# Kernel optimization log

Hardware: AMD Instinct MI355X
Metric: run time of the kernel (lower is better)

## Reference

```python
import jax, jax.numpy as jnp
import numpy as np

N_NODES = 10000


def _sage_pool(h, src, dst, Wp, bp, Ws, Wn, b):
    # DGL SAGEConv 'pool': m = relu(fc_pool(h_src)); neigh = max over in-edges;
    # out = fc_self(h_dst) + fc_neigh(neigh) + bias. Zero-in-degree nodes get 0 neigh.
    m = jax.nn.relu(h @ Wp + bp)                      # [N, d_in] node-level transform
    neigh = jax.ops.segment_max(m[src], dst, num_segments=N_NODES)  # [N, d_in]
    neigh = jnp.where(jnp.isfinite(neigh), neigh, 0.0)  # empty segments filled -inf -> 0
    return h @ Ws + neigh @ Wn + b


def setup_inputs() -> dict:
    key = jax.random.key(0)
    ks = jax.random.split(key, 20)
    dims = [(960, 512), (512, 512), (512, 1)]
    inp = {
        "h": jax.random.normal(ks[0], (N_NODES, 960), dtype=jnp.float32),
        "src": jax.random.randint(ks[1], (160000,), 0, N_NODES),
        "dst": jax.random.randint(ks[2], (160000,), 0, N_NODES),
    }
    ki = 3
    for l, (di, do) in enumerate(dims):
        inp[f"Wp{l}"] = jax.random.normal(ks[ki + 0], (di, di), dtype=jnp.float32) * 0.02
        inp[f"bp{l}"] = jnp.zeros((di,), dtype=jnp.float32)
        inp[f"Ws{l}"] = jax.random.normal(ks[ki + 1], (di, do), dtype=jnp.float32) * 0.02
        inp[f"Wn{l}"] = jax.random.normal(ks[ki + 2], (di, do), dtype=jnp.float32) * 0.02
        inp[f"b{l}"] = jnp.zeros((do,), dtype=jnp.float32)
        ki += 3
    return inp


def reference(h, src, dst,
              Wp0, bp0, Ws0, Wn0, b0,
              Wp1, bp1, Ws1, Wn1, b1,
              Wp2, bp2, Ws2, Wn2, b2):
    # layer 0: 960 -> 512, relu (dropout = identity in eval)
    x = jax.nn.relu(_sage_pool(h, src, dst, Wp0, bp0, Ws0, Wn0, b0))
    # layer 1: 512 -> 512, relu
    x = jax.nn.relu(_sage_pool(x, src, dst, Wp1, bp1, Ws1, Wn1, b1))
    # layer 2: 512 -> 1, sigmoid, squeeze -> per-node prediction
    x = _sage_pool(x, src, dst, Wp2, bp2, Ws2, Wn2, b2)
    return jax.nn.sigmoid(x).squeeze(-1)  # [N]
```

## Files before the change

### kernel.cpp

```cpp
#include <hip/hip_runtime.h>
#include <stdint.h>

#define NN 10000
#define NE 160000
#define MPAD 10112
#define MTILES 79

typedef unsigned short u16;
typedef float f32x4 __attribute__((ext_vector_type(4)));
typedef short short8 __attribute__((ext_vector_type(8)));
typedef __bf16 bf16x8 __attribute__((ext_vector_type(8)));
typedef unsigned short u16x4 __attribute__((ext_vector_type(4)));
typedef unsigned short u16x8 __attribute__((ext_vector_type(8)));

__device__ __forceinline__ float bf2f(u16 u) {
  union { unsigned u; float f; } c; c.u = ((unsigned)u) << 16; return c.f;
}
__device__ __forceinline__ u16 f2bf(float f) {
  union { float f; unsigned u; } c; c.f = f;
  return (u16)((c.u + 0x7FFFu + ((c.u >> 16) & 1u)) >> 16);
}

__device__ __forceinline__ void gld_lds16(void* lds, const void* g) {
  __builtin_amdgcn_global_load_lds(
      (const unsigned int __attribute__((address_space(1)))*)g,
      (unsigned int __attribute__((address_space(3)))*)lds, 16, 0, 0);
}

__global__ __launch_bounds__(256) void deg_count(const int* __restrict__ dst, int* __restrict__ deg) {
  int e = blockIdx.x * 256 + threadIdx.x;
  if (e < NE) atomicAdd(&deg[dst[e]], 1);
}

__global__ __launch_bounds__(256) void scan_off(const int* __restrict__ deg,
                                                int* __restrict__ roff, int* __restrict__ cur) {
  __shared__ int sdeg[10240];
  __shared__ int part[256];
  const int t = threadIdx.x;
  for (int k = t; k < NN; k += 256) sdeg[k] = deg[k];
  for (int k = NN + t; k < 10240; k += 256) sdeg[k] = 0;
  __syncthreads();
  const int CH = 40;
  int s = 0;
#pragma unroll
  for (int i = 0; i < CH; ++i) s += sdeg[t * CH + i];
  part[t] = s; __syncthreads();
  for (int off = 1; off < 256; off <<= 1) {
    int v = (t >= off) ? part[t - off] : 0;
    __syncthreads(); part[t] += v; __syncthreads();
  }
  int run = (t == 0) ? 0 : part[t - 1];
#pragma unroll
  for (int i = 0; i < CH; ++i) {
    const int idx = t * CH + i;
    const int d = sdeg[idx];
    sdeg[idx] = run;
    run += d;
  }
  __syncthreads();
  for (int k = t; k < NN; k += 256) { const int v = sdeg[k]; roff[k] = v; cur[k] = v; }
  if (t == 255) roff[NN] = NE;
}

__global__ __launch_bounds__(256) void fill_csr(const int* __restrict__ src, const int* __restrict__ dst,
                                                int* __restrict__ cur, int* __restrict__ esrc) {
  int e = blockIdx.x * 256 + threadIdx.x;
  if (e < NE) {
    int p = atomicAdd(&cur[dst[e]], 1);
    esrc[p] = src[e];
  }
}

__global__ __launch_bounds__(256) void convert_h(const float* __restrict__ h, u16* __restrict__ hbf,
                                                 int* __restrict__ deg) {
  if (blockIdx.x < 40) {
    const int z = blockIdx.x * 256 + threadIdx.x;
    if (z < NN) deg[z] = 0;
  }
  const size_t i = (size_t)(blockIdx.x * 256 + threadIdx.x) * 4;
  if (i >= (size_t)MPAD * 960) return;
  u16x4 o;
  if (i < (size_t)NN * 960) {
    float4 v = *(const float4*)(h + i);
    o[0] = f2bf(v.x); o[1] = f2bf(v.y); o[2] = f2bf(v.z); o[3] = f2bf(v.w);
  } else {
    o[0] = 0; o[1] = 0; o[2] = 0; o[3] = 0;
  }
  *(u16x4*)(hbf + i) = o;
}

struct WDesc { const float* in; u16* out; int R, C, Cpad, ldo, koff; };
struct WPack { WDesc d[7]; };

__global__ __launch_bounds__(256) void transpose_all(WPack p) {
  const WDesc w = p.d[blockIdx.z];
  const int cb = blockIdx.x * 32, rb = blockIdx.y * 32;
  if (cb >= w.Cpad || rb >= w.R) return;
  __shared__ float tile[32][33];
  const int tx = threadIdx.x & 31, ty = threadIdx.x >> 5;
  for (int i = ty; i < 32; i += 8) {
    int r = rb + i, c = cb + tx;
    tile[i][tx] = (r < w.R && c < w.C) ? w.in[(size_t)r * w.C + c] : 0.f;
  }
  __syncthreads();
  for (int i = ty; i < 32; i += 8) {
    int c = cb + i, r = rb + tx;
    if (c < w.Cpad && r < w.R) w.out[(size_t)c * w.ldo + w.koff + r] = f2bf(tile[tx][i]);
  }
}

template<int TM, int TN, int MINW>
__global__ __launch_bounds__(512, MINW) void gemm3(
    const u16* __restrict__ A0, int lda0,
    const u16* __restrict__ A1, int lda1, int ksplit,
    const u16* __restrict__ B,
    const float* __restrict__ bias, int nbias,
    u16* __restrict__ Cb, int ldcb,
    int K, int act, int tiles_n) {
  constexpr int TR = TM + TN;
  constexpr int NC = TR * 128 / (512 * 16);
  constexpr int WCOLS = 4;
  constexpr int WN = TN / WCOLS;
  constexpr int NJ = WN / 16;
  constexpr int MT = MPAD / TM;
  __shared__ __align__(16) u16 S0[TR * 64];
  __shared__ __align__(16) u16 S1[TR * 64];
  const int tid = threadIdx.x;
  const int wave = tid >> 6, lane = tid & 63;

  const int nwg = tiles_n * MT;
  const int orig = blockIdx.x + blockIdx.y * tiles_n;
  const int q = nwg >> 3, r8 = nwg & 7;
  const int xcd = orig & 7, idx = orig >> 3;
  const int wg = (xcd < r8 ? xcd * (q + 1) : r8 * (q + 1) + (xcd - r8) * q) + idx;
  const int tm = (wg / tiles_n) * TM;
  const int tn = (wg % tiles_n) * TN;

  const int wr = (wave / WCOLS) * 64;
  const int wc = (wave % WCOLS) * WN;
  const int fr = lane & 15, fq = lane >> 4;
  const int sr8 = lane >> 3;
  const int sslot = lane & 7;
  f32x4 acc[4][NJ] = {};

  auto stage = [&](u16* Sw, int kk) {
#pragma unroll
    for (int c = 0; c < NC; ++c) {
      const int row = c * 64 + wave * 8 + sr8;
      const int gs = (sslot ^ (row & 7)) * 8;
      const void* g;
      if (c < NC * TM / TR) {
        g = (kk < ksplit)
            ? (const void*)&A0[(size_t)(tm + row) * lda0 + kk + gs]
            : (const void*)&A1[(size_t)(tm + row) * lda1 + (kk - ksplit) + gs];
      } else {
        g = (const void*)&B[(size_t)(tn + row - TM) * (size_t)K + kk + gs];
      }
      gld_lds16(&Sw[(c * 64 + wave * 8) * 64], g);
    }
  };

  const int nsteps = K >> 6;
  stage(S0, 0);
  stage(S1, 64);
  for (int base = 0; base < nsteps; base += 2) {
#pragma unroll
    for (int ph = 0; ph < 2; ++ph) {
      const int t = base + ph;
      if (t >= nsteps) break;
      u16* Sr = (ph == 0) ? S0 : S1;
      if (t + 1 < nsteps) {
        asm volatile("s_waitcnt vmcnt(%0)" :: "i"(NC) : "memory");
      } else {
        asm volatile("s_waitcnt vmcnt(0)" ::: "memory");
      }
      __builtin_amdgcn_s_barrier();
      __builtin_amdgcn_sched_barrier(0);
      short8 af[4][2], bfr[2][NJ];
#pragma unroll
      for (int i = 0; i < 4; ++i) {
        const int r = wr + i * 16 + fr;
#pragma unroll
        for (int kc = 0; kc < 2; ++kc)
          af[i][kc] = *(const short8*)&Sr[r * 64 + ((((kc << 2) | fq) ^ (r & 7)) << 3)];
      }
#pragma unroll
      for (int j = 0; j < NJ; ++j) {
        const int r = TM + wc + j * 16 + fr;
#pragma unroll
        for (int kc = 0; kc < 2; ++kc)
          bfr[kc][j] = *(const short8*)&Sr[r * 64 + ((((kc << 2) | fq) ^ (r & 7)) << 3)];
      }
      asm volatile("s_waitcnt lgkmcnt(0)" ::: "memory");
      __builtin_amdgcn_sched_barrier(0);
      __builtin_amdgcn_s_barrier();
      if (t + 2 < nsteps) stage(Sr, (t + 2) << 6);
      __builtin_amdgcn_s_setprio(1);
#pragma unroll
      for (int kc = 0; kc < 2; ++kc)
#pragma unroll
        for (int i = 0; i < 4; ++i)
#pragma unroll
          for (int j = 0; j < NJ; ++j)
            acc[i][j] = __builtin_amdgcn_mfma_f32_16x16x32_bf16(
                __builtin_bit_cast(bf16x8, af[i][kc]), __builtin_bit_cast(bf16x8, bfr[kc][j]),
                acc[i][j], 0, 0, 0);
      __builtin_amdgcn_s_setprio(0);
      __builtin_amdgcn_sched_barrier(0);
    }
  }

  const int cr = fq * 4, cc = fr;
#pragma unroll
  for (int i = 0; i < 4; ++i)
#pragma unroll
    for (int j = 0; j < NJ; ++j) {
      const int col = tn + wc + j * 16 + cc;
      const float bv = (col < nbias) ? bias[col] : 0.f;
#pragma unroll
      for (int r = 0; r < 4; ++r) {
        const int row = tm + wr + i * 16 + cr + r;
        float v = acc[i][j][r] + bv;
        if (act) v = fmaxf(v, 0.f);
        Cb[(size_t)row * ldcb + col] = f2bf(v);
      }
    }
}

template<int CW>
__global__ __launch_bounds__(256) void aggregate_xcd(
    const u16* __restrict__ m, int ldm, const int* __restrict__ roff,
    const int* __restrict__ esrc, u16* __restrict__ neigh, int ldn) {
  constexpr int TPN = CW / 8;
  constexpr int NPB = 256 / TPN;
  const int chunk = blockIdx.x & 7;
  const int node = (blockIdx.x >> 3) * NPB + threadIdx.x / TPN;
  if (node >= NN) return;
  const int fi = chunk * CW + (threadIdx.x % TPN) * 8;
  const int beg = roff[node], end = roff[node + 1];
  u16x8 a;
#pragma unroll
  for (int i = 0; i < 8; ++i) a[i] = 0;
  for (int e = beg; e < end; ++e) {
    const u16* row = m + (size_t)esrc[e] * ldm;
    u16x8 v = *(const u16x8*)(row + fi);
#pragma unroll
    for (int i = 0; i < 8; ++i) a[i] = (v[i] > a[i]) ? v[i] : a[i];
  }
  *(u16x8*)(neigh + (size_t)node * ldn + fi) = a;
}

__global__ __launch_bounds__(256) void agg_final(
    const u16* __restrict__ m, const int* __restrict__ roff,
    const int* __restrict__ esrc, const u16* __restrict__ x,
    const float* __restrict__ ws, const float* __restrict__ wn,
    const float* __restrict__ b, float* __restrict__ out) {
  const int wave = threadIdx.x >> 6, lane = threadIdx.x & 63;
  const int n = blockIdx.x * 4 + wave;
  if (n >= NN) return;
  const int f = lane * 8;
  const int beg = roff[n], end = roff[n + 1];
  u16x8 a;
#pragma unroll
  for (int i = 0; i < 8; ++i) a[i] = 0;
  for (int e = beg; e < end; ++e) {
    u16x8 v = *(const u16x8*)(m + (size_t)esrc[e] * 512 + f);
#pragma unroll
    for (int i = 0; i < 8; ++i) a[i] = (v[i] > a[i]) ? v[i] : a[i];
  }
  const u16x8 xv = *(const u16x8*)(x + (size_t)n * 512 + f);
  float s = 0.f;
#pragma unroll
  for (int i = 0; i < 8; ++i)
    s += bf2f(xv[i]) * ws[f + i] + bf2f(a[i]) * wn[f + i];
#pragma unroll
  for (int o = 32; o > 0; o >>= 1) s += __shfl_xor(s, o);
  if (lane == 0) out[n] = 1.f / (1.f + expf(-(s + b[0])));
}

extern "C" void kernel_launch(void* const* d_in, const int* in_sizes, int n_in,
                              void* d_out, int out_size, void* d_ws, size_t ws_size,
                              hipStream_t stream) {
  const float* h   = (const float*)d_in[0];
  const int*   src = (const int*)d_in[1];
  const int*   dst = (const int*)d_in[2];
  const float* Wp0 = (const float*)d_in[3];
  const float* bp0 = (const float*)d_in[4];
  const float* Ws0 = (const float*)d_in[5];
  const float* Wn0 = (const float*)d_in[6];
  const float* b0  = (const float*)d_in[7];
  const float* Wp1 = (const float*)d_in[8];
  const float* bp1 = (const float*)d_in[9];
  const float* Ws1 = (const float*)d_in[10];
  const float* Wn1 = (const float*)d_in[11];
  const float* b1  = (const float*)d_in[12];
  const float* Wp2 = (const float*)d_in[13];
  const float* bp2 = (const float*)d_in[14];
  const float* Ws2 = (const float*)d_in[15];
  const float* Wn2 = (const float*)d_in[16];
  const float* b2  = (const float*)d_in[17];
  float* out = (float*)d_out;

  char* ws = (char*)d_ws;
  size_t off = 0;
  auto alloc = [&](size_t n) { char* p = ws + off; off = (off + n + 255) & ~(size_t)255; return p; };
  u16* hbf   = (u16*)alloc((size_t)MPAD * 960 * 2);
  u16* x1    = (u16*)alloc((size_t)MPAD * 512 * 2);
  u16* x2    = (u16*)alloc((size_t)MPAD * 512 * 2);
  u16* mbuf  = (u16*)alloc((size_t)MPAD * 1024 * 2);
  u16* nbuf  = (u16*)alloc((size_t)MPAD * 1024 * 2);
  u16* WpT0  = (u16*)alloc((size_t)1024 * 960 * 2);
  u16* Bcat0 = (u16*)alloc((size_t)512 * 1920 * 2);
  u16* WpT1  = (u16*)alloc((size_t)512 * 512 * 2);
  u16* Bcat1 = (u16*)alloc((size_t)512 * 1024 * 2);
  u16* WpT2  = (u16*)alloc((size_t)512 * 512 * 2);
  int* deg   = (int*)alloc(NN * 4);
  int* roff  = (int*)alloc((NN + 1) * 4);
  int* curp  = (int*)alloc(NN * 4);
  int* esrc  = (int*)alloc(NE * 4);

  convert_h<<<(MPAD * 960 / 4) / 256, 256, 0, stream>>>(h, hbf, deg);
  deg_count<<<NE / 256, 256, 0, stream>>>(dst, deg);
  scan_off<<<1, 256, 0, stream>>>(deg, roff, curp);
  fill_csr<<<NE / 256, 256, 0, stream>>>(src, dst, curp, esrc);

  WPack wp;
  wp.d[0] = {Wp0, WpT0,  960, 960, 1024,  960,   0};
  wp.d[1] = {Ws0, Bcat0, 960, 512,  512, 1920,   0};
  wp.d[2] = {Wn0, Bcat0, 960, 512,  512, 1920, 960};
  wp.d[3] = {Wp1, WpT1,  512, 512,  512,  512,   0};
  wp.d[4] = {Ws1, Bcat1, 512, 512,  512, 1024,   0};
  wp.d[5] = {Wn1, Bcat1, 512, 512,  512, 1024, 512};
  wp.d[6] = {Wp2, WpT2,  512, 512,  512,  512,   0};
  transpose_all<<<dim3(32, 30, 7), 256, 0, stream>>>(wp);

  gemm3<128, 128, 4><<<dim3(8, 79), 512, 0, stream>>>(
      hbf, 960, hbf, 960, 960, WpT0, bp0, 960, mbuf, 1024, 960, 1, 8);
  aggregate_xcd<128><<<5000, 256, 0, stream>>>(mbuf, 1024, roff, esrc, nbuf, 1024);
  gemm3<128, 128, 4><<<dim3(4, 79), 512, 0, stream>>>(
      hbf, 960, nbuf, 1024, 960, Bcat0, b0, 512, x1, 512, 1920, 1, 4);

  gemm3<128, 128, 4><<<dim3(4, 79), 512, 0, stream>>>(
      x1, 512, x1, 512, 512, WpT1, bp1, 512, mbuf, 512, 512, 1, 4);
  aggregate_xcd<64><<<2504, 256, 0, stream>>>(mbuf, 512, roff, esrc, nbuf, 512);
  gemm3<128, 128, 4><<<dim3(4, 79), 512, 0, stream>>>(
      x1, 512, nbuf, 512, 512, Bcat1, b1, 512, x2, 512, 1024, 1, 4);

  gemm3<128, 128, 4><<<dim3(4, 79), 512, 0, stream>>>(
      x2, 512, x2, 512, 512, WpT2, bp2, 512, mbuf, 512, 512, 1, 4);
  agg_final<<<2500, 256, 0, stream>>>(mbuf, roff, esrc, x2, Ws2, Wn2, b2, out);
}
```

Before: 228.7 us.

## Fuse self-projection into pool GEMM and fold CSR fill into transpose kernel

Layers 0 and 1 now fold the self term h@Ws into the same GEMM as the pool transform by concatenating Wp and Ws along N. The extra column tiles write fp32 partials, and the neighbour GEMM adds them back in its epilogue, so that GEMM's K shrinks to just the neighbour dimension. The CSR fill is merged into transpose_all as an extra z-slice, which removes one launch. The cost is fp32 partial buffers that must be written and read again, plus a wider first GEMM grid.

```diff
diff --git a/kernel.cpp b/kernel.cpp
--- a/kernel.cpp
+++ b/kernel.cpp
@@ -62,15 +62,6 @@
   if (t == 255) roff[NN] = NE;
 }
 
-__global__ __launch_bounds__(256) void fill_csr(const int* __restrict__ src, const int* __restrict__ dst,
-                                                int* __restrict__ cur, int* __restrict__ esrc) {
-  int e = blockIdx.x * 256 + threadIdx.x;
-  if (e < NE) {
-    int p = atomicAdd(&cur[dst[e]], 1);
-    esrc[p] = src[e];
-  }
-}
-
 __global__ __launch_bounds__(256) void convert_h(const float* __restrict__ h, u16* __restrict__ hbf,
                                                  int* __restrict__ deg) {
   if (blockIdx.x < 40) {
@@ -90,9 +81,17 @@
 }
 
 struct WDesc { const float* in; u16* out; int R, C, Cpad, ldo, koff; };
-struct WPack { WDesc d[7]; };
+struct WPack { WDesc d[7]; const int* src; const int* dst; int* cur; int* esrc; };
 
 __global__ __launch_bounds__(256) void transpose_all(WPack p) {
+  if (blockIdx.z == 7) {
+    int e = (blockIdx.y * 32 + blockIdx.x) * 256 + threadIdx.x;
+    if (e < NE) {
+      int pos = atomicAdd(&p.cur[p.dst[e]], 1);
+      p.esrc[pos] = p.src[e];
+    }
+    return;
+  }
   const WDesc w = p.d[blockIdx.z];
   const int cb = blockIdx.x * 32, rb = blockIdx.y * 32;
   if (cb >= w.Cpad || rb >= w.R) return;
@@ -116,6 +115,8 @@
     const u16* __restrict__ B,
     const float* __restrict__ bias, int nbias,
     u16* __restrict__ Cb, int ldcb,
+    float* __restrict__ Cf, int ldcf, int nsplit,
+    const float* __restrict__ Cin, int ldcin,
     int K, int act, int tiles_n) {
   constexpr int TR = TM + TN;
   constexpr int NC = TR * 128 / (512 * 16);
@@ -211,20 +212,35 @@
   }
 
   const int cr = fq * 4, cc = fr;
-#pragma unroll
-  for (int i = 0; i < 4; ++i)
-#pragma unroll
-    for (int j = 0; j < NJ; ++j) {
-      const int col = tn + wc + j * 16 + cc;
-      const float bv = (col < nbias) ? bias[col] : 0.f;
-#pragma unroll
-      for (int r = 0; r < 4; ++r) {
-        const int row = tm + wr + i * 16 + cr + r;
-        float v = acc[i][j][r] + bv;
-        if (act) v = fmaxf(v, 0.f);
-        Cb[(size_t)row * ldcb + col] = f2bf(v);
-      }
-    }
+  if (tn < nsplit) {
+#pragma unroll
+    for (int i = 0; i < 4; ++i)
+#pragma unroll
+      for (int j = 0; j < NJ; ++j) {
+        const int col = tn + wc + j * 16 + cc;
+        const float bv = (col < nbias) ? bias[col] : 0.f;
+#pragma unroll
+        for (int r = 0; r < 4; ++r) {
+          const int row = tm + wr + i * 16 + cr + r;
+          float v = acc[i][j][r] + bv;
+          if (Cin) v += Cin[(size_t)row * ldcin + col];
+          if (act) v = fmaxf(v, 0.f);
+          Cb[(size_t)row * ldcb + col] = f2bf(v);
+        }
+      }
+  } else {
+#pragma unroll
+    for (int i = 0; i < 4; ++i)
+#pragma unroll
+      for (int j = 0; j < NJ; ++j) {
+        const int col = tn - nsplit + wc + j * 16 + cc;
+#pragma unroll
+        for (int r = 0; r < 4; ++r) {
+          const int row = tm + wr + i * 16 + cr + r;
+          Cf[(size_t)row * ldcf + col] = acc[i][j][r];
+        }
+      }
+  }
 }
 
 template<int CW>
@@ -309,10 +325,12 @@
   u16* x2    = (u16*)alloc((size_t)MPAD * 512 * 2);
   u16* mbuf  = (u16*)alloc((size_t)MPAD * 1024 * 2);
   u16* nbuf  = (u16*)alloc((size_t)MPAD * 1024 * 2);
-  u16* WpT0  = (u16*)alloc((size_t)1024 * 960 * 2);
-  u16* Bcat0 = (u16*)alloc((size_t)512 * 1920 * 2);
-  u16* WpT1  = (u16*)alloc((size_t)512 * 512 * 2);
-  u16* Bcat1 = (u16*)alloc((size_t)512 * 1024 * 2);
+  float* xa0 = (float*)alloc((size_t)MPAD * 512 * 4);
+  float* xa1 = (float*)alloc((size_t)MPAD * 512 * 4);
+  u16* Wcat0 = (u16*)alloc((size_t)1536 * 960 * 2);
+  u16* WnT0  = (u16*)alloc((size_t)512 * 960 * 2);
+  u16* Wcat1 = (u16*)alloc((size_t)1024 * 512 * 2);
+  u16* WnT1  = (u16*)alloc((size_t)512 * 512 * 2);
   u16* WpT2  = (u16*)alloc((size_t)512 * 512 * 2);
   int* deg   = (int*)alloc(NN * 4);
   int* roff  = (int*)alloc((NN + 1) * 4);
@@ -322,31 +340,36 @@
   convert_h<<<(MPAD * 960 / 4) / 256, 256, 0, stream>>>(h, hbf, deg);
   deg_count<<<NE / 256, 256, 0, stream>>>(dst, deg);
   scan_off<<<1, 256, 0, stream>>>(deg, roff, curp);
-  fill_csr<<<NE / 256, 256, 0, stream>>>(src, dst, curp, esrc);
 
   WPack wp;
-  wp.d[0] = {Wp0, WpT0,  960, 960, 1024,  960,   0};
-  wp.d[1] = {Ws0, Bcat0, 960, 512,  512, 1920,   0};
-  wp.d[2] = {Wn0, Bcat0, 960, 512,  512, 1920, 960};
-  wp.d[3] = {Wp1, WpT1,  512, 512,  512,  512,   0};
-  wp.d[4] = {Ws1, Bcat1, 512, 512,  512, 1024,   0};
-  wp.d[5] = {Wn1, Bcat1, 512, 512,  512, 1024, 512};
-  wp.d[6] = {Wp2, WpT2,  512, 512,  512,  512,   0};
-  transpose_all<<<dim3(32, 30, 7), 256, 0, stream>>>(wp);
-
-  gemm3<128, 128, 4><<<dim3(8, 79), 512, 0, stream>>>(
-      hbf, 960, hbf, 960, 960, WpT0, bp0, 960, mbuf, 1024, 960, 1, 8);
+  wp.d[0] = {Wp0, Wcat0,              960, 960, 1024, 960, 0};
+  wp.d[1] = {Ws0, Wcat0 + 1024 * 960, 960, 512,  512, 960, 0};
+  wp.d[2] = {Wn0, WnT0,               960, 512,  512, 960, 0};
+  wp.d[3] = {Wp1, Wcat1,              512, 512,  512, 512, 0};
+  wp.d[4] = {Ws1, Wcat1 + 512 * 512,  512, 512,  512, 512, 0};
+  wp.d[5] = {Wn1, WnT1,               512, 512,  512, 512, 0};
+  wp.d[6] = {Wp2, WpT2,               512, 512,  512, 512, 0};
+  wp.src = src; wp.dst = dst; wp.cur = curp; wp.esrc = esrc;
+  transpose_all<<<dim3(32, 30, 8), 256, 0, stream>>>(wp);
+
+  gemm3<128, 128, 4><<<dim3(12, 79), 512, 0, stream>>>(
+      hbf, 960, hbf, 960, 960, Wcat0, bp0, 960,
+      mbuf, 1024, xa0, 512, 1024, nullptr, 0, 960, 1, 12);
   aggregate_xcd<128><<<5000, 256, 0, stream>>>(mbuf, 1024, roff, esrc, nbuf, 1024);
   gemm3<128, 128, 4><<<dim3(4, 79), 512, 0, stream>>>(
-      hbf, 960, nbuf, 1024, 960, Bcat0, b0, 512, x1, 512, 1920, 1, 4);
-
-  gemm3<128, 128, 4><<<dim3(4, 79), 512, 0, stream>>>(
-      x1, 512, x1, 512, 512, WpT1, bp1, 512, mbuf, 512, 512, 1, 4);
+      nbuf, 1024, nbuf, 1024, 960, WnT0, b0, 512,
+      x1, 512, nullptr, 0, 512, xa0, 512, 960, 1, 4);
+
+  gemm3<128, 128, 4><<<dim3(8, 79), 512, 0, stream>>>(
+      x1, 512, x1, 512, 512, Wcat1, bp1, 512,
+      mbuf, 512, xa1, 512, 512, nullptr, 0, 512, 1, 8);
   aggregate_xcd<64><<<2504, 256, 0, stream>>>(mbuf, 512, roff, esrc, nbuf, 512);
   gemm3<128, 128, 4><<<dim3(4, 79), 512, 0, stream>>>(
-      x1, 512, nbuf, 512, 512, Bcat1, b1, 512, x2, 512, 1024, 1, 4);
+      nbuf, 512, nbuf, 512, 512, WnT1, b1, 512,
+      x2, 512, nullptr, 0, 512, xa1, 512, 512, 1, 4);
 
   gemm3<128, 128, 4><<<dim3(4, 79), 512, 0, stream>>>(
-      x2, 512, x2, 512, 512, WpT2, bp2, 512, mbuf, 512, 512, 1, 4);
+      x2, 512, x2, 512, 512, WpT2, bp2, 512,
+      mbuf, 512, nullptr, 0, 512, nullptr, 0, 512, 1, 4);
   agg_final<<<2500, 256, 0, stream>>>(mbuf, roff, esrc, x2, Ws2, Wn2, b2, out);
 }
```

Result: slower. 245.9 us (+7.5%).
